# Performance work log

Measured on AMD Instinct MI355X. Metric: run time of the kernel, lower is better.

Reference implementation:

```python
import jax, jax.numpy as jnp
import numpy as np

D_MODEL = 768
HEAD_SIZE = 64

def setup_inputs() -> dict:
    key = jax.random.key(0)
    ks = jax.random.split(key, 7)
    B, S = 8, 2048
    x = jax.random.normal(ks[0], (B, S, D_MODEL), dtype=jnp.float32)
    s = 1.0 / np.sqrt(D_MODEL)
    Wq = jax.random.uniform(ks[1], (D_MODEL, HEAD_SIZE), jnp.float32, -s, s)
    bq = jnp.zeros((HEAD_SIZE,), jnp.float32)
    Wk = jax.random.uniform(ks[2], (D_MODEL, HEAD_SIZE), jnp.float32, -s, s)
    bk = jnp.zeros((HEAD_SIZE,), jnp.float32)
    Wv = jax.random.uniform(ks[3], (D_MODEL, HEAD_SIZE), jnp.float32, -s, s)
    bv = jnp.zeros((HEAD_SIZE,), jnp.float32)
    return {"x": x, "Wq": Wq, "bq": bq, "Wk": Wk, "bk": bk, "Wv": Wv, "bv": bv}

def reference(x, Wq, bq, Wk, bk, Wv, bv):
    # Single attention head: softmax(Q K^T / sqrt(head_size)) V
    q = jnp.einsum('bsd,dh->bsh', x, Wq) + bq  # [B,S,H]
    k = jnp.einsum('bsd,dh->bsh', x, Wk) + bk
    v = jnp.einsum('bsd,dh->bsh', x, Wv) + bv
    scale = 1.0 / jnp.sqrt(jnp.array(HEAD_SIZE, dtype=x.dtype))
    scores = jnp.einsum('bqh,bkh->bqk', q, k) * scale  # [B,S,S]
    attn = jax.nn.softmax(scores, axis=-1)
    out = jnp.einsum('bqk,bkh->bqh', attn, v)  # [B,S,H]
    return out
```

## Files before the change

### kernel.cpp

```cpp
#include <hip/hip_runtime.h>
#include <math.h>

#define D_MODEL 768
#define HS 64
#define BATCH 8
#define SEQ 2048
#define SCALE 0.125f
#define KSPLIT 8
#define KCHUNK (SEQ / KSPLIT)

typedef _Float16 half_t;
typedef __attribute__((ext_vector_type(8))) _Float16 half8;
typedef __attribute__((ext_vector_type(4))) float floatx4;

typedef const __attribute__((address_space(1))) void gas_void;
typedef __attribute__((address_space(3))) void las_void;
__device__ __forceinline__ void gl_lds16(const void* g, void* l) {
    __builtin_amdgcn_global_load_lds((gas_void*)g, (las_void*)l, 16, 0, 0);
}
__device__ __forceinline__ void waitcnt_all() {
    __builtin_amdgcn_s_waitcnt(0);
}

__global__ __launch_bounds__(256)
void wconv_kernel(const float* __restrict__ Wq, const float* __restrict__ Wk,
                  const float* __restrict__ Wv, half_t* __restrict__ Wt)
{
    int m = blockIdx.x >> 6;
    int h = blockIdx.x & 63;
    const float* W = (m == 0) ? Wq : ((m == 1) ? Wk : Wv);
    half_t* dst = Wt + (size_t)blockIdx.x * D_MODEL;
    for (int k = threadIdx.x; k < D_MODEL; k += 256)
        dst[k] = (half_t)W[(size_t)k * HS + h];
}

__global__ __launch_bounds__(256)
void proj_kernel(const float* __restrict__ x, const half_t* __restrict__ Wt,
                 const float* __restrict__ bq, const float* __restrict__ bk,
                 const float* __restrict__ bv,
                 half_t* __restrict__ Qh, half_t* __restrict__ Kh,
                 half_t* __restrict__ Vt)
{
    __shared__ __align__(16) half_t xs[2][64 * 64];
    __shared__ __align__(16) half_t wt[2][192 * 64];

    const int tid = threadIdx.x;
    const int w = tid >> 6;
    const int lane = tid & 63;
    const int l15 = lane & 15;
    const int quad = lane >> 4;
    const long row0 = (long)blockIdx.x * 64;

    floatx4 acc[4][3];
#pragma unroll
    for (int i = 0; i < 4; ++i)
#pragma unroll
        for (int j = 0; j < 3; ++j) acc[i][j] = (floatx4){0.f, 0.f, 0.f, 0.f};

    float4 xA[4], xB[4];
    half8  wA[6], wB[6];

    auto loadx = [&](int k0, float4 (&v)[4]) {
#pragma unroll
        for (int i = 0; i < 2; ++i) {
            int idx = i * 256 + tid;
            int r = idx >> 3, sc = idx & 7;
            int cg = sc ^ (r & 7);
            const float* p = x + (row0 + r) * D_MODEL + k0 + cg * 8;
            v[i * 2]     = *(const float4*)p;
            v[i * 2 + 1] = *(const float4*)(p + 4);
        }
    };
    auto loadw = [&](int k0, half8 (&wr)[6]) {
#pragma unroll
        for (int i = 0; i < 6; ++i) {
            int idx = i * 256 + tid;
            int r = idx >> 3, sc = idx & 7;
            int cg = sc ^ (r & 7);
            wr[i] = *(const half8*)(Wt + (size_t)r * D_MODEL + k0 + cg * 8);
        }
    };

    auto step = [&](int it, float4 (&xc)[4], half8 (&wc)[6],
                    float4 (&xn)[4], half8 (&wn)[6], int p) {
#pragma unroll
        for (int i = 0; i < 2; ++i) {
            float4 a = xc[i * 2], b = xc[i * 2 + 1];
            half8 xh = (half8){(half_t)a.x, (half_t)a.y, (half_t)a.z, (half_t)a.w,
                               (half_t)b.x, (half_t)b.y, (half_t)b.z, (half_t)b.w};
            *(half8*)&xs[p][(i * 256 + tid) * 8] = xh;
        }
#pragma unroll
        for (int i = 0; i < 6; ++i)
            *(half8*)&wt[p][(i * 256 + tid) * 8] = wc[i];
        __syncthreads();
        int kn = (it + 1 < 12) ? (it + 1) * 64 : 0;
        loadx(kn, xn);
        loadw(kn, wn);
#pragma unroll
        for (int kst = 0; kst < 2; ++kst) {
            half8 af[4];
#pragma unroll
            for (int mt = 0; mt < 4; ++mt) {
                int r = mt * 16 + l15;
                int slot = (kst * 4 + quad) ^ (r & 7);
                af[mt] = *(const half8*)&xs[p][r * 64 + slot * 8];
            }
#pragma unroll
            for (int nt = 0; nt < 3; ++nt) {
                int r = w * 48 + nt * 16 + l15;
                int slot = (kst * 4 + quad) ^ (r & 7);
                half8 bf = *(const half8*)&wt[p][r * 64 + slot * 8];
#pragma unroll
                for (int mt = 0; mt < 4; ++mt)
                    acc[mt][nt] = __builtin_amdgcn_mfma_f32_16x16x32_f16(
                        af[mt], bf, acc[mt][nt], 0, 0, 0);
            }
        }
    };

    loadx(0, xA);
    loadw(0, wA);
#pragma unroll
    for (int it = 0; it < 12; it += 2) {
        step(it,     xA, wA, xB, wB, 0);
        step(it + 1, xB, wB, xA, wA, 1);
    }

#pragma unroll
    for (int nt = 0; nt < 3; ++nt) {
        int nbase = w * 48 + nt * 16;
        int mm = nbase >> 6;
        int h = (nbase + l15) & 63;
        const float* bias = (mm == 0) ? bq : ((mm == 1) ? bk : bv);
        float bval = bias[h];
#pragma unroll
        for (int mt = 0; mt < 4; ++mt)
#pragma unroll
            for (int r = 0; r < 4; ++r) {
                long R = row0 + mt * 16 + quad * 4 + r;
                half_t hv = (half_t)(acc[mt][nt][r] + bval);
                if (mm == 0)      Qh[R * HS + h] = hv;
                else if (mm == 1) Kh[R * HS + h] = hv;
                else {
                    long bb = R >> 11, s = R & 2047;
                    Vt[(bb * HS + h) * SEQ + s] = hv;
                }
            }
    }
}

__global__ __launch_bounds__(128)
void attn_kernel(const half_t* __restrict__ Qh, const half_t* __restrict__ Kh,
                 const half_t* __restrict__ Vt,
                 half_t* __restrict__ Opart, float* __restrict__ lpart)
{
    __shared__ __align__(16) half_t ks[64 * 64];
    __shared__ __align__(16) half_t vs[64 * 64];
    __shared__ __align__(16) half_t ps[2][16][72];

    const int tid = threadIdx.x;
    const int w = tid >> 6;
    const int lane = tid & 63;
    const int l15 = lane & 15;
    const int quad = lane >> 4;
    const int b = blockIdx.y;
    const int q0 = blockIdx.x * 128 + w * 64;
    const int kh = blockIdx.z;
    const int kk_begin = kh * KCHUNK;

    const half_t* Kb = Kh + (size_t)b * SEQ * HS;
    const half_t* Vb = Vt + (size_t)b * HS * SEQ;

    half8 qf[4][2];
#pragma unroll
    for (int mt = 0; mt < 4; ++mt)
#pragma unroll
        for (int kst = 0; kst < 2; ++kst) {
            half8 q = *(const half8*)(Qh + ((size_t)b * SEQ + q0 + mt * 16 + l15) * HS
                                      + kst * 32 + quad * 8);
#pragma unroll
            for (int j = 0; j < 8; ++j) q[j] = q[j] * (half_t)SCALE;
            qf[mt][kst] = q;
        }

    floatx4 oacc[4][4];
    float lsum[4][4];
#pragma unroll
    for (int mt = 0; mt < 4; ++mt) {
#pragma unroll
        for (int nt = 0; nt < 4; ++nt) oacc[mt][nt] = (floatx4){0.f, 0.f, 0.f, 0.f};
#pragma unroll
        for (int r = 0; r < 4; ++r) lsum[mt][r] = 0.f;
    }

    for (int it = 0; it < KCHUNK / 64; ++it) {
        const int kk0 = kk_begin + it * 64;
        __syncthreads();
#pragma unroll
        for (int i = 0; i < 4; ++i) {
            int idx = i * 128 + tid;
            int r = idx >> 3, sc = idx & 7;
            int cg = sc ^ (r & 7);
            gl_lds16(Kb + (size_t)(kk0 + r) * HS + cg * 8, ks + idx * 8);
            gl_lds16(Vb + (size_t)r * SEQ + kk0 + cg * 8, vs + idx * 8);
        }
        waitcnt_all();
        __syncthreads();

        half8 vf[4][2];
#pragma unroll
        for (int nt = 0; nt < 4; ++nt)
#pragma unroll
            for (int kst = 0; kst < 2; ++kst) {
                int r = nt * 16 + l15;
                int slot = (kst * 4 + quad) ^ (r & 7);
                vf[nt][kst] = *(const half8*)&vs[r * 64 + slot * 8];
            }

#pragma unroll
        for (int h2 = 0; h2 < 2; ++h2) {
            floatx4 sacc[2][4];
#pragma unroll
            for (int mtl = 0; mtl < 2; ++mtl)
#pragma unroll
                for (int nt = 0; nt < 4; ++nt) sacc[mtl][nt] = (floatx4){0.f, 0.f, 0.f, 0.f};
#pragma unroll
            for (int nt = 0; nt < 4; ++nt)
#pragma unroll
                for (int kst = 0; kst < 2; ++kst) {
                    int r = nt * 16 + l15;
                    int slot = (kst * 4 + quad) ^ (r & 7);
                    half8 kf = *(const half8*)&ks[r * 64 + slot * 8];
#pragma unroll
                    for (int mtl = 0; mtl < 2; ++mtl)
                        sacc[mtl][nt] = __builtin_amdgcn_mfma_f32_16x16x32_f16(
                            qf[h2 * 2 + mtl][kst], kf, sacc[mtl][nt], 0, 0, 0);
                }

#pragma unroll
            for (int mtl = 0; mtl < 2; ++mtl) {
                int mt = h2 * 2 + mtl;
#pragma unroll
                for (int nt = 0; nt < 4; ++nt)
#pragma unroll
                    for (int r = 0; r < 4; ++r) {
                        float pv = __expf(sacc[mtl][nt][r]);
                        lsum[mt][r] += pv;
                        ps[w][quad * 4 + r][nt * 16 + l15] = (half_t)pv;
                    }
                half8 pfr[2];
#pragma unroll
                for (int kst = 0; kst < 2; ++kst)
                    pfr[kst] = *(const half8*)&ps[w][l15][kst * 32 + quad * 8];
#pragma unroll
                for (int nt = 0; nt < 4; ++nt)
#pragma unroll
                    for (int kst = 0; kst < 2; ++kst)
                        oacc[mt][nt] = __builtin_amdgcn_mfma_f32_16x16x32_f16(
                            pfr[kst], vf[nt][kst], oacc[mt][nt], 0, 0, 0);
            }
        }
    }

#pragma unroll
    for (int mt = 0; mt < 4; ++mt)
#pragma unroll
        for (int r = 0; r < 4; ++r) {
            float s = lsum[mt][r];
            s += __shfl_xor(s, 1);
            s += __shfl_xor(s, 2);
            s += __shfl_xor(s, 4);
            s += __shfl_xor(s, 8);
            lsum[mt][r] = s;
        }

    size_t obase = ((size_t)kh * BATCH + b) * SEQ * HS;
#pragma unroll
    for (int mt = 0; mt < 4; ++mt)
#pragma unroll
        for (int nt = 0; nt < 4; ++nt)
#pragma unroll
            for (int r = 0; r < 4; ++r) {
                int row = q0 + mt * 16 + quad * 4 + r;
                Opart[obase + (size_t)row * HS + nt * 16 + l15] = (half_t)oacc[mt][nt][r];
            }
    if (l15 == 0) {
#pragma unroll
        for (int mt = 0; mt < 4; ++mt)
#pragma unroll
            for (int r = 0; r < 4; ++r) {
                int row = q0 + mt * 16 + quad * 4 + r;
                lpart[((size_t)kh * BATCH + b) * SEQ + row] = lsum[mt][r];
            }
    }
}

__global__ __launch_bounds__(256)
void combine_kernel(const half_t* __restrict__ Opart, const float* __restrict__ lpart,
                    float* __restrict__ out)
{
    const size_t NT = (size_t)BATCH * SEQ * HS;
    const size_t BS = (size_t)BATCH * SEQ;
    size_t e0 = ((size_t)blockIdx.x * 256 + threadIdx.x) * 8;
    size_t row = e0 / HS;
    float o[8] = {0, 0, 0, 0, 0, 0, 0, 0};
    float l = 0.f;
#pragma unroll
    for (int i = 0; i < KSPLIT; ++i) {
        half8 oi = *(const half8*)(Opart + (size_t)i * NT + e0);
#pragma unroll
        for (int j = 0; j < 8; ++j) o[j] += (float)oi[j];
        l += lpart[(size_t)i * BS + row];
    }
    float inv = 1.f / l;
    float4 a = {o[0] * inv, o[1] * inv, o[2] * inv, o[3] * inv};
    float4 c = {o[4] * inv, o[5] * inv, o[6] * inv, o[7] * inv};
    *(float4*)(out + e0) = a;
    *(float4*)(out + e0 + 4) = c;
}

extern "C" void kernel_launch(void* const* d_in, const int* in_sizes, int n_in,
                              void* d_out, int out_size, void* d_ws, size_t ws_size,
                              hipStream_t stream) {
    const float* x  = (const float*)d_in[0];
    const float* Wq = (const float*)d_in[1];
    const float* bq = (const float*)d_in[2];
    const float* Wk = (const float*)d_in[3];
    const float* bk = (const float*)d_in[4];
    const float* Wv = (const float*)d_in[5];
    const float* bv = (const float*)d_in[6];
    float* out = (float*)d_out;

    const size_t per = (size_t)BATCH * SEQ * HS;
    half_t* Qh = (half_t*)d_ws;
    half_t* Kh = Qh + per;
    half_t* Vt = Kh + per;
    half_t* Wt = Vt + per;
    half_t* Opart = Wt + 3 * HS * D_MODEL;
    float*  lpart = (float*)(Opart + (size_t)KSPLIT * per);

    wconv_kernel<<<dim3(3 * HS), dim3(256), 0, stream>>>(Wq, Wk, Wv, Wt);
    proj_kernel<<<dim3(BATCH * SEQ / 64), dim3(256), 0, stream>>>(
        x, Wt, bq, bk, bv, Qh, Kh, Vt);
    attn_kernel<<<dim3(SEQ / 128, BATCH, KSPLIT), dim3(128), 0, stream>>>(
        Qh, Kh, Vt, Opart, lpart);
    combine_kernel<<<dim3((BATCH * SEQ * HS) / (256 * 8)), dim3(256), 0, stream>>>(
        Opart, lpart, out);
}
```

Measured before the change: 141.2 us.

## Fuse split-K combine into attention kernel via last-block atomic counter

Removes the separate combine kernel launch. Each attention block increments a per-(batch, query-block) counter after writing its partial output. The last of the KSPLIT blocks to finish reduces the partials and writes the normalized fp32 output. This saves a kernel launch and its scheduling gap. In exchange it adds fences, an atomic and a serialized tail reduction inside the final blocks, with counters reset by the weight-conversion kernel.

```diff
diff --git a/kernel.cpp b/kernel.cpp
--- a/kernel.cpp
+++ b/kernel.cpp
@@ -24,8 +24,11 @@
 
 __global__ __launch_bounds__(256)
 void wconv_kernel(const float* __restrict__ Wq, const float* __restrict__ Wk,
-                  const float* __restrict__ Wv, half_t* __restrict__ Wt)
+                  const float* __restrict__ Wv, half_t* __restrict__ Wt,
+                  int* __restrict__ cnt)
 {
+    if (blockIdx.x == 0 && threadIdx.x < BATCH * (SEQ / 128))
+        cnt[threadIdx.x] = 0;
     int m = blockIdx.x >> 6;
     int h = blockIdx.x & 63;
     const float* W = (m == 0) ? Wq : ((m == 1) ? Wk : Wv);
@@ -153,11 +156,13 @@
 __global__ __launch_bounds__(128)
 void attn_kernel(const half_t* __restrict__ Qh, const half_t* __restrict__ Kh,
                  const half_t* __restrict__ Vt,
-                 half_t* __restrict__ Opart, float* __restrict__ lpart)
+                 half_t* __restrict__ Opart, float* __restrict__ lpart,
+                 int* __restrict__ cnt, float* __restrict__ out)
 {
     __shared__ __align__(16) half_t ks[64 * 64];
     __shared__ __align__(16) half_t vs[64 * 64];
     __shared__ __align__(16) half_t ps[2][16][72];
+    __shared__ int is_last;
 
     const int tid = threadIdx.x;
     const int w = tid >> 6;
@@ -165,7 +170,8 @@
     const int l15 = lane & 15;
     const int quad = lane >> 4;
     const int b = blockIdx.y;
-    const int q0 = blockIdx.x * 128 + w * 64;
+    const int qblk = blockIdx.x;
+    const int q0 = qblk * 128 + w * 64;
     const int kh = blockIdx.z;
     const int kk_begin = kh * KCHUNK;
 
@@ -294,30 +300,38 @@
                 lpart[((size_t)kh * BATCH + b) * SEQ + row] = lsum[mt][r];
             }
     }
-}
-
-__global__ __launch_bounds__(256)
-void combine_kernel(const half_t* __restrict__ Opart, const float* __restrict__ lpart,
-                    float* __restrict__ out)
-{
-    const size_t NT = (size_t)BATCH * SEQ * HS;
-    const size_t BS = (size_t)BATCH * SEQ;
-    size_t e0 = ((size_t)blockIdx.x * 256 + threadIdx.x) * 8;
-    size_t row = e0 / HS;
-    float o[8] = {0, 0, 0, 0, 0, 0, 0, 0};
-    float l = 0.f;
-#pragma unroll
-    for (int i = 0; i < KSPLIT; ++i) {
-        half8 oi = *(const half8*)(Opart + (size_t)i * NT + e0);
-#pragma unroll
-        for (int j = 0; j < 8; ++j) o[j] += (float)oi[j];
-        l += lpart[(size_t)i * BS + row];
-    }
-    float inv = 1.f / l;
-    float4 a = {o[0] * inv, o[1] * inv, o[2] * inv, o[3] * inv};
-    float4 c = {o[4] * inv, o[5] * inv, o[6] * inv, o[7] * inv};
-    *(float4*)(out + e0) = a;
-    *(float4*)(out + e0 + 4) = c;
+
+    __threadfence();
+    if (tid == 0)
+        is_last = (atomicAdd(&cnt[b * (SEQ / 128) + qblk], 1) == KSPLIT - 1);
+    __syncthreads();
+    if (is_last) {
+        __threadfence();
+        const size_t NT = (size_t)BATCH * SEQ * HS;
+        const size_t BS = (size_t)BATCH * SEQ;
+        const int rbase = qblk * 128;
+#pragma unroll
+        for (int c = 0; c < 8; ++c) {
+            int eidx = (c * 128 + tid) * 8;
+            int row = rbase + (eidx >> 6);
+            int col = eidx & 63;
+            size_t e0 = ((size_t)b * SEQ + row) * HS + col;
+            float o[8] = {0, 0, 0, 0, 0, 0, 0, 0};
+            float l = 0.f;
+#pragma unroll
+            for (int i = 0; i < KSPLIT; ++i) {
+                half8 oi = *(const half8*)(Opart + (size_t)i * NT + e0);
+#pragma unroll
+                for (int j = 0; j < 8; ++j) o[j] += (float)oi[j];
+                l += lpart[(size_t)i * BS + (size_t)b * SEQ + row];
+            }
+            float inv = 1.f / l;
+            float4 a = {o[0] * inv, o[1] * inv, o[2] * inv, o[3] * inv};
+            float4 d = {o[4] * inv, o[5] * inv, o[6] * inv, o[7] * inv};
+            *(float4*)(out + e0) = a;
+            *(float4*)(out + e0 + 4) = d;
+        }
+    }
 }
 
 extern "C" void kernel_launch(void* const* d_in, const int* in_sizes, int n_in,
@@ -339,12 +353,11 @@
     half_t* Wt = Vt + per;
     half_t* Opart = Wt + 3 * HS * D_MODEL;
     float*  lpart = (float*)(Opart + (size_t)KSPLIT * per);
-
-    wconv_kernel<<<dim3(3 * HS), dim3(256), 0, stream>>>(Wq, Wk, Wv, Wt);
+    int*    cnt   = (int*)(lpart + (size_t)KSPLIT * BATCH * SEQ);
+
+    wconv_kernel<<<dim3(3 * HS), dim3(256), 0, stream>>>(Wq, Wk, Wv, Wt, cnt);
     proj_kernel<<<dim3(BATCH * SEQ / 64), dim3(256), 0, stream>>>(
         x, Wt, bq, bk, bv, Qh, Kh, Vt);
     attn_kernel<<<dim3(SEQ / 128, BATCH, KSPLIT), dim3(128), 0, stream>>>(
-        Qh, Kh, Vt, Opart, lpart);
-    combine_kernel<<<dim3((BATCH * SEQ * HS) / (256 * 8)), dim3(256), 0, stream>>>(
-        Opart, lpart, out);
-}
+        Qh, Kh, Vt, Opart, lpart, cnt, out);
+}
```

New measurement: 216.2 us. 53.1% more time.
